# Performance work log

Hardware: AMD Instinct MI355X
Metric: run time of the kernel (lower is better)

The kernel has to match this reference:

```python
import jax, jax.numpy as jnp
import numpy as np

D_MODEL = 1024
NUM_HEADS = 16
HEAD_DIM = D_MODEL // NUM_HEADS


def setup_inputs() -> dict:
    key = jax.random.key(0)
    k_x, k_wqkv, k_bqkv, k_wout, k_bout = jax.random.split(key, 5)
    B, S = 2, 2048
    x = jax.random.normal(k_x, (B, S, D_MODEL), dtype=jnp.float32)
    # haiku Linear: y = x @ W + b, W shape [in, out]
    init_scale = 1.0 / np.sqrt(D_MODEL)
    W_qkv = jax.random.normal(k_wqkv, (D_MODEL, 3 * D_MODEL), dtype=jnp.float32) * init_scale
    b_qkv = jnp.zeros((3 * D_MODEL,), dtype=jnp.float32)
    W_out = jax.random.normal(k_wout, (D_MODEL, D_MODEL), dtype=jnp.float32) * init_scale
    b_out = jnp.zeros((D_MODEL,), dtype=jnp.float32)
    return {"x": x, "W_qkv": W_qkv, "b_qkv": b_qkv, "W_out": W_out, "b_out": b_out}


def reference(x, W_qkv, b_qkv, W_out, b_out):
    B, S, _ = x.shape
    qkv = x @ W_qkv + b_qkv                      # [B, S, 3*D]
    q, k, v = jnp.split(qkv, 3, axis=-1)         # each [B, S, D]
    # [B, S, D] -> [B, H, S, Hd]
    def heads(t):
        return t.reshape(B, S, NUM_HEADS, HEAD_DIM).transpose(0, 2, 1, 3)
    q, k, v = heads(q), heads(k), heads(v)
    scale = jnp.sqrt(jnp.float32(HEAD_DIM)).astype(x.dtype)
    attn = jnp.einsum('bhqd,bhkd->bhqk', q, k) / scale   # [B, H, S, S]
    attn = jax.nn.softmax(attn, axis=-1)
    out = jnp.einsum('bhqk,bhkd->bhqd', attn, v)          # [B, H, S, Hd]
    out = out.transpose(0, 2, 1, 3).reshape(B, S, D_MODEL)
    return out @ W_out + b_out
```

## Files before the change

### kernel.cpp

```cpp
#include <hip/hip_runtime.h>
#include <stdint.h>


#define BATCH 2
#define SEQ 2048
#define DM 1024
#define NH 16
#define HD 64
#define M_TOT 4096
#define QSCALE 0.18033688011112042f

typedef __bf16 bf16x8 __attribute__((ext_vector_type(8)));
typedef __bf16 bf16x4 __attribute__((ext_vector_type(4)));
typedef float  f32x4  __attribute__((ext_vector_type(4)));

__device__ __forceinline__ void gld_lds16(const void* g, void* l) {
    __builtin_amdgcn_global_load_lds(
        (const __attribute__((address_space(1))) uint32_t*)g,
        (__attribute__((address_space(3))) uint32_t*)l, 16, 0, 0);
}

__device__ __forceinline__ int swz(int r, int c) {
    return r * 64 + ((((c >> 3) ^ (r & 7))) << 3) + (c & 7);
}

__launch_bounds__(256)
__global__ void split_x_kernel(const float* __restrict__ x, __bf16* __restrict__ xs)
{
    const int i  = blockIdx.x * 256 + threadIdx.x;
    const int m  = i >> 8;
    const int c4 = (i & 255) * 4;
    float4 v = *reinterpret_cast<const float4*>(&x[(size_t)m * DM + c4]);
    float a[4] = {v.x, v.y, v.z, v.w};
    bf16x4 hi, lo;
    #pragma unroll
    for (int j = 0; j < 4; ++j) {
        __bf16 h = (__bf16)a[j];
        hi[j] = h;
        lo[j] = (__bf16)(a[j] - (float)h);
    }
    *reinterpret_cast<bf16x4*>(&xs[(size_t)m * (2*DM) + c4]) = hi;
    *reinterpret_cast<bf16x4*>(&xs[(size_t)m * (2*DM) + DM + c4]) = lo;
}

__launch_bounds__(256)
__global__ void split_wt_kernel(const float* __restrict__ W, __bf16* __restrict__ Wt, int N)
{
    __shared__ float T[64][69];
    const int tid = threadIdx.x;
    const int k0 = blockIdx.x * 64, n0 = blockIdx.y * 64;

    {
        const int kr = tid >> 4, c4 = (tid & 15) * 4;
        #pragma unroll
        for (int i = 0; i < 4; ++i) {
            float4 v = *reinterpret_cast<const float4*>(
                &W[(size_t)(k0 + kr + 16 * i) * N + n0 + c4]);
            *reinterpret_cast<float4*>(&T[kr + 16 * i][c4]) = v;
        }
    }
    __syncthreads();
    {
        const int n = tid >> 2, kc = (tid & 3) * 16;
        __bf16 hi[16], lo[16];
        #pragma unroll
        for (int j = 0; j < 16; ++j) {
            float v = T[kc + j][n];
            __bf16 h = (__bf16)v;
            hi[j] = h;
            lo[j] = (__bf16)(v - (float)h);
        }
        const size_t ro = (size_t)(n0 + n) * (2*DM) + k0 + kc;
        *reinterpret_cast<bf16x8*>(&Wt[ro])          = *reinterpret_cast<bf16x8*>(&hi[0]);
        *reinterpret_cast<bf16x8*>(&Wt[ro + 8])      = *reinterpret_cast<bf16x8*>(&hi[8]);
        *reinterpret_cast<bf16x8*>(&Wt[ro + DM])     = *reinterpret_cast<bf16x8*>(&lo[0]);
        *reinterpret_cast<bf16x8*>(&Wt[ro + DM + 8]) = *reinterpret_cast<bf16x8*>(&lo[8]);
    }
}

__launch_bounds__(256)
__global__ void gemm_qkv_kernel(const __bf16* __restrict__ A,
                                const __bf16* __restrict__ Bt,
                                const float* __restrict__ bias,
                                __bf16* __restrict__ qs,
                                __bf16* __restrict__ khi_g,
                                __bf16* __restrict__ klo_g,
                                __bf16* __restrict__ vt_g)
{
    __shared__ __align__(16) __bf16 pool[18432];
    __bf16* As = pool;
    __bf16* Bs = pool + 4096;

    const int tid  = threadIdx.x;
    const int w    = tid >> 6;
    const int lane = tid & 63;
    const int n16  = lane & 15;
    const int quad = lane >> 4;
    const int bm = blockIdx.x * 128, bn = blockIdx.y * 128;
    const int wm = (w & 1) * 64,     wn = (w >> 1) * 64;

    const int srow = tid >> 2, sc = (tid & 3) * 8;
    const __bf16* Ar = A  + (size_t)(bm + srow) * (2*DM) + sc;
    const __bf16* Br = Bt + (size_t)(bn + srow) * (2*DM) + sc;

    f32x4 acc[4][4] = {};

    for (int kb = 0; kb < 3 * DM; kb += 32) {
        const int a_k = (kb < DM)     ? kb : kb - DM;
        const int b_k = (kb < 2 * DM) ? kb : kb - 2 * DM;
        __syncthreads();
        gld_lds16(Ar + a_k,                    &As[(size_t)tid * 8]);
        gld_lds16(Ar + a_k + (size_t)64*2*DM,  &As[(size_t)(256 + tid) * 8]);
        gld_lds16(Br + b_k,                    &Bs[(size_t)tid * 8]);
        gld_lds16(Br + b_k + (size_t)64*2*DM,  &Bs[(size_t)(256 + tid) * 8]);
        __syncthreads();

        bf16x8 af[4], bfr[4];
        #pragma unroll
        for (int i = 0; i < 4; ++i)
            af[i] = *reinterpret_cast<const bf16x8*>(&As[(wm + i*16 + n16) * 32 + quad * 8]);
        #pragma unroll
        for (int j = 0; j < 4; ++j)
            bfr[j] = *reinterpret_cast<const bf16x8*>(&Bs[(wn + j*16 + n16) * 32 + quad * 8]);
        #pragma unroll
        for (int i = 0; i < 4; ++i)
            #pragma unroll
            for (int j = 0; j < 4; ++j)
                acc[i][j] = __builtin_amdgcn_mfma_f32_16x16x32_bf16(af[i], bfr[j], acc[i][j], 0, 0, 0);
    }

    const int colb = bn + wn;
    const int part = colb >> 10;
    const int hh   = (colb & 1023) >> 6;
    const int brow = bm + wm;
    const int b    = brow >> 11;
    const int s0   = brow & 2047;
    const int bh   = b * NH + hh;
    const int kt   = s0 >> 6;
    const size_t tb = ((size_t)bh * 32 + kt) * 4096;

    float bv[4];
    #pragma unroll
    for (int j = 0; j < 4; ++j) bv[j] = bias[colb + j * 16 + n16];

    __bf16* scrH = pool + w * 4608;
    __bf16* scrL = scrH + 2304;
    const int lr = lane & 31, hc = lane >> 5;

    __syncthreads();

    #pragma unroll
    for (int p = 0; p < 2; ++p) {
        if (part == 2) {
            #pragma unroll
            for (int jj = 0; jj < 2; ++jj) {
                const int j = 2 * p + jj;
                #pragma unroll
                for (int i = 0; i < 4; ++i) {
                    bf16x4 v4;
                    #pragma unroll
                    for (int r = 0; r < 4; ++r)
                        v4[r] = (__bf16)(acc[i][j][r] + bv[j]);
                    *reinterpret_cast<bf16x4*>(
                        &scrH[(jj * 16 + n16) * 72 + i * 16 + quad * 4]) = v4;
                }
            }
        } else {
            #pragma unroll
            for (int ii = 0; ii < 2; ++ii) {
                const int i = 2 * p + ii;
                #pragma unroll
                for (int j = 0; j < 4; ++j) {
                    #pragma unroll
                    for (int r = 0; r < 4; ++r) {
                        float val = acc[i][j][r] + bv[j];
                        if (part == 0) val *= QSCALE;
                        __bf16 h = (__bf16)val;
                        const int so = (ii * 16 + quad * 4 + r) * 72 + j * 16 + n16;
                        scrH[so] = h;
                        scrL[so] = (__bf16)(val - (float)h);
                    }
                }
            }
        }
        __syncthreads();

        if (part == 0) {
            const size_t qbase = ((size_t)bh * SEQ + s0 + 32 * p + lr) * 128;
            #pragma unroll
            for (int t = 0; t < 4; ++t) {
                const int ch = hc * 4 + t;
                *reinterpret_cast<bf16x8*>(&qs[qbase + ch * 8]) =
                    *reinterpret_cast<const bf16x8*>(&scrH[lr * 72 + ch * 8]);
                *reinterpret_cast<bf16x8*>(&qs[qbase + 64 + ch * 8]) =
                    *reinterpret_cast<const bf16x8*>(&scrL[lr * 72 + ch * 8]);
            }
        } else if (part == 1) {
            const int kr = 32 * p + lr;
            #pragma unroll
            for (int t = 0; t < 4; ++t) {
                const int ch = hc * 4 + t;
                const int src = (ch ^ (lr & 7)) * 8;
                *reinterpret_cast<bf16x8*>(&khi_g[tb + kr * 64 + ch * 8]) =
                    *reinterpret_cast<const bf16x8*>(&scrH[lr * 72 + src]);
                *reinterpret_cast<bf16x8*>(&klo_g[tb + kr * 64 + ch * 8]) =
                    *reinterpret_cast<const bf16x8*>(&scrL[lr * 72 + src]);
            }
        } else {
            const int d = 32 * p + lr;
            #pragma unroll
            for (int t = 0; t < 4; ++t) {
                const int ch = hc * 4 + t;
                const int src = (ch ^ (lr & 7)) * 8;
                *reinterpret_cast<bf16x8*>(&vt_g[tb + d * 64 + ch * 8]) =
                    *reinterpret_cast<const bf16x8*>(&scrH[lr * 72 + src]);
            }
        }
        __syncthreads();
    }
}

__launch_bounds__(256)
__global__ void gemm_out_kernel(const __bf16* __restrict__ A,
                                const __bf16* __restrict__ Bt,
                                const float* __restrict__ bias,
                                float* __restrict__ out)
{
    __shared__ __align__(16) __bf16 As[128 * 32];
    __shared__ __align__(16) __bf16 Bs[64 * 32];

    const int tid  = threadIdx.x;
    const int w    = tid >> 6;
    const int lane = tid & 63;
    const int n16  = lane & 15;
    const int quad = lane >> 4;
    const int bm = blockIdx.x * 128, bn = blockIdx.y * 64;
    const int wm = (w & 1) * 64,     wn = (w >> 1) * 32;

    const int srow = tid >> 2, sc = (tid & 3) * 8;
    const __bf16* Ar = A  + (size_t)(bm + srow) * (2*DM) + sc;
    const __bf16* Br = Bt + (size_t)(bn + srow) * (2*DM) + sc;

    f32x4 acc[4][2] = {};

    for (int kb = 0; kb < 3 * DM; kb += 32) {
        const int a_k = (kb < DM)     ? kb : kb - DM;
        const int b_k = (kb < 2 * DM) ? kb : kb - 2 * DM;
        __syncthreads();
        gld_lds16(Ar + a_k,                    &As[(size_t)tid * 8]);
        gld_lds16(Ar + a_k + (size_t)64*2*DM,  &As[(size_t)(256 + tid) * 8]);
        gld_lds16(Br + b_k,                    &Bs[(size_t)tid * 8]);
        __syncthreads();

        bf16x8 af[4], bfr[2];
        #pragma unroll
        for (int i = 0; i < 4; ++i)
            af[i] = *reinterpret_cast<const bf16x8*>(&As[(wm + i*16 + n16) * 32 + quad * 8]);
        #pragma unroll
        for (int j = 0; j < 2; ++j)
            bfr[j] = *reinterpret_cast<const bf16x8*>(&Bs[(wn + j*16 + n16) * 32 + quad * 8]);
        #pragma unroll
        for (int i = 0; i < 4; ++i)
            #pragma unroll
            for (int j = 0; j < 2; ++j)
                acc[i][j] = __builtin_amdgcn_mfma_f32_16x16x32_bf16(af[i], bfr[j], acc[i][j], 0, 0, 0);
    }

    #pragma unroll
    for (int j = 0; j < 2; ++j) {
        const int col = bn + wn + j * 16 + n16;
        const float bvv = bias[col];
        #pragma unroll
        for (int i = 0; i < 4; ++i) {
            const int row0 = bm + wm + i * 16 + quad * 4;
            #pragma unroll
            for (int r = 0; r < 4; ++r)
                out[(size_t)(row0 + r) * DM + col] = acc[i][j][r] + bvv;
        }
    }
}

__launch_bounds__(512)
__global__ void flash_attn_dma_kernel(const __bf16* __restrict__ qs,
                                      const __bf16* __restrict__ khi_g,
                                      const __bf16* __restrict__ klo_g,
                                      const __bf16* __restrict__ vt_g,
                                      __bf16* __restrict__ ctx2)
{
    __shared__ __align__(16) __bf16 Khi[4096];
    __shared__ __align__(16) __bf16 Klo[4096];
    __shared__ __align__(16) __bf16 Vt [4096];
    __shared__ __align__(16) __bf16 Ps [8192];

    const int tid  = threadIdx.x;
    const int w    = tid >> 6;
    const int lane = tid & 63;
    const int n16  = lane & 15;
    const int quad = lane >> 4;
    const int bid  = blockIdx.x;
    const int bh = (bid & 7) * 4 + (bid >> 7);
    const int qt = (bid >> 3) & 15;

    const size_t qrow = ((size_t)bh * SEQ + qt * 128 + w * 16 + n16) * 128;
    bf16x8 qh[2], ql[2];
    #pragma unroll
    for (int s2 = 0; s2 < 2; ++s2) {
        qh[s2] = *reinterpret_cast<const bf16x8*>(&qs[qrow + s2 * 32 + quad * 8]);
        ql[s2] = *reinterpret_cast<const bf16x8*>(&qs[qrow + 64 + s2 * 32 + quad * 8]);
    }

    f32x4 o[4] = {};
    float l_lane = 0.f;

    const int prow = w * 16 + n16;

    for (int kt = 0; kt < 32; ++kt) {
        const size_t tb = ((size_t)bh * 32 + kt) * 4096;
        __syncthreads();
        #pragma unroll
        for (int t = 0; t < 3; ++t) {
            const int ch = w * 3 + t;
            const int arr = ch >> 3, sub = ch & 7;
            const int eo = sub * 512 + lane * 8;
            const __bf16* g = (arr == 0 ? khi_g : arr == 1 ? klo_g : vt_g) + tb + eo;
            __bf16* l = (arr == 0 ? Khi : arr == 1 ? Klo : Vt) + eo;
            gld_lds16(g, l);
        }
        __syncthreads();

        f32x4 st[4] = {};
        #pragma unroll
        for (int kg = 0; kg < 4; ++kg) {
            const int r = kg * 16 + n16;
            #pragma unroll
            for (int s2 = 0; s2 < 2; ++s2) {
                const int off = r * 64 + (((s2 * 4 + quad) ^ (r & 7)) << 3);
                bf16x8 kh = *reinterpret_cast<const bf16x8*>(&Khi[off]);
                bf16x8 kl = *reinterpret_cast<const bf16x8*>(&Klo[off]);
                st[kg] = __builtin_amdgcn_mfma_f32_16x16x32_bf16(kh, qh[s2], st[kg], 0, 0, 0);
                st[kg] = __builtin_amdgcn_mfma_f32_16x16x32_bf16(kh, ql[s2], st[kg], 0, 0, 0);
                st[kg] = __builtin_amdgcn_mfma_f32_16x16x32_bf16(kl, qh[s2], st[kg], 0, 0, 0);
            }
        }

        float lp[4];
        #pragma unroll
        for (int kg = 0; kg < 4; ++kg) {
            f32x4 pp;
            #pragma unroll
            for (int r2 = 0; r2 < 4; ++r2)
                pp[r2] = exp2f(st[kg][r2]);
            st[kg] = pp;
            lp[kg] = (pp[0] + pp[1]) + (pp[2] + pp[3]);
        }
        l_lane += (lp[0] + lp[1]) + (lp[2] + lp[3]);

        #pragma unroll
        for (int kg = 0; kg < 4; ++kg) {
            bf16x4 p4;
            #pragma unroll
            for (int r2 = 0; r2 < 4; ++r2) p4[r2] = (__bf16)st[kg][r2];
            const int ch = kg * 2 + (quad >> 1);
            const int off = prow * 64 + ((ch ^ (prow & 7)) << 3) + (quad & 1) * 4;
            *reinterpret_cast<bf16x4*>(&Ps[off]) = p4;
        }

        bf16x8 pa[2];
        #pragma unroll
        for (int s2 = 0; s2 < 2; ++s2)
            pa[s2] = *reinterpret_cast<const bf16x8*>(
                &Ps[prow * 64 + (((s2 * 4 + quad) ^ (prow & 7)) << 3)]);
        #pragma unroll
        for (int c = 0; c < 4; ++c) {
            const int vr = c * 16 + n16;
            #pragma unroll
            for (int s2 = 0; s2 < 2; ++s2) {
                bf16x8 vb = *reinterpret_cast<const bf16x8*>(
                    &Vt[vr * 64 + (((s2 * 4 + quad) ^ (vr & 7)) << 3)]);
                o[c] = __builtin_amdgcn_mfma_f32_16x16x32_bf16(pa[s2], vb, o[c], 0, 0, 0);
            }
        }
    }

    l_lane += __shfl_xor(l_lane, 16, 64);
    l_lane += __shfl_xor(l_lane, 32, 64);

    const int b = bh >> 4, hh = bh & 15;
    #pragma unroll
    for (int r2 = 0; r2 < 4; ++r2) {
        const float l = __shfl(l_lane, (quad << 4) + quad * 4 + r2, 64);
        const float linv = 1.0f / l;
        const int srow = qt * 128 + w * 16 + quad * 4 + r2;
        const size_t rowoff = (size_t)(b * SEQ + srow) * (2*DM);
        #pragma unroll
        for (int c = 0; c < 4; ++c) {
            const int col = hh * HD + c * 16 + n16;
            float v = o[c][r2] * linv;
            __bf16 h = (__bf16)v;
            ctx2[rowoff + col] = h;
            ctx2[rowoff + DM + col] = (__bf16)(v - (float)h);
        }
    }
}

extern "C" void kernel_launch(void* const* d_in, const int* in_sizes, int n_in,
                              void* d_out, int out_size, void* d_ws, size_t ws_size,
                              hipStream_t stream)
{
    const float* x    = (const float*)d_in[0];
    const float* Wqkv = (const float*)d_in[1];
    const float* bqkv = (const float*)d_in[2];
    const float* Wout = (const float*)d_in[3];
    const float* bout = (const float*)d_in[4];
    float* out = (float*)d_out;

    char* ws = (char*)d_ws;
    __bf16* xs   = (__bf16*)(ws);
    __bf16* ctx2 = xs;
    __bf16* wqt  = (__bf16*)(ws + (size_t)16 * 1024 * 1024);
    __bf16* wot  = (__bf16*)(ws + (size_t)28 * 1024 * 1024);
    __bf16* qsb  = (__bf16*)(ws + (size_t)32 * 1024 * 1024);
    __bf16* khi  = (__bf16*)(ws + (size_t)48 * 1024 * 1024);
    __bf16* klo  = (__bf16*)(ws + (size_t)56 * 1024 * 1024);
    __bf16* vt   = (__bf16*)(ws + (size_t)64 * 1024 * 1024);

    split_x_kernel<<<dim3(M_TOT * (DM / 4) / 256), 256, 0, stream>>>(x, xs);
    split_wt_kernel<<<dim3(DM / 64, (3 * DM) / 64), 256, 0, stream>>>(Wqkv, wqt, 3 * DM);
    split_wt_kernel<<<dim3(DM / 64, DM / 64), 256, 0, stream>>>(Wout, wot, DM);

    gemm_qkv_kernel<<<dim3(M_TOT / 128, (3 * DM) / 128), 256, 0, stream>>>(
        xs, wqt, bqkv, qsb, khi, klo, vt);
    flash_attn_dma_kernel<<<dim3(512), 512, 0, stream>>>(qsb, khi, klo, vt, ctx2);
    gemm_out_kernel<<<dim3(M_TOT / 128, DM / 64), 256, 0, stream>>>(
        ctx2, wot, bout, out);
}
```

Baseline: 306.1 us.

## Give each attention wave four query groups and merge prep kernels into one launch

The flash attention kernel drops from 8 to 2 waves per block, and each wave now handles 64 query rows (four 16-row groups). Every K and V fragment read from LDS is reused across four MFMA groups, which cuts LDS read traffic per MFMA. The cost is much higher register pressure (accumulators and Q fragments for four groups), fewer waves per CU, and more DMA issues per wave. The three preprocessing kernels (x split and both weight transpose/splits) are also merged into one launch to save launch overhead.

```diff
diff --git a/kernel.cpp b/kernel.cpp
--- a/kernel.cpp
+++ b/kernel.cpp
@@ -25,30 +25,40 @@
 }
 
 __launch_bounds__(256)
-__global__ void split_x_kernel(const float* __restrict__ x, __bf16* __restrict__ xs)
-{
-    const int i  = blockIdx.x * 256 + threadIdx.x;
-    const int m  = i >> 8;
-    const int c4 = (i & 255) * 4;
-    float4 v = *reinterpret_cast<const float4*>(&x[(size_t)m * DM + c4]);
-    float a[4] = {v.x, v.y, v.z, v.w};
-    bf16x4 hi, lo;
-    #pragma unroll
-    for (int j = 0; j < 4; ++j) {
-        __bf16 h = (__bf16)a[j];
-        hi[j] = h;
-        lo[j] = (__bf16)(a[j] - (float)h);
-    }
-    *reinterpret_cast<bf16x4*>(&xs[(size_t)m * (2*DM) + c4]) = hi;
-    *reinterpret_cast<bf16x4*>(&xs[(size_t)m * (2*DM) + DM + c4]) = lo;
-}
-
-__launch_bounds__(256)
-__global__ void split_wt_kernel(const float* __restrict__ W, __bf16* __restrict__ Wt, int N)
+__global__ void prep_kernel(const float* __restrict__ x,
+                            const float* __restrict__ Wqkv,
+                            const float* __restrict__ Wout,
+                            __bf16* __restrict__ xs,
+                            __bf16* __restrict__ wqt,
+                            __bf16* __restrict__ wot)
 {
     __shared__ float T[64][69];
     const int tid = threadIdx.x;
-    const int k0 = blockIdx.x * 64, n0 = blockIdx.y * 64;
+    const int blk = blockIdx.x;
+
+    if (blk < 4096) {
+        const int i  = blk * 256 + tid;
+        const int m  = i >> 8;
+        const int c4 = (i & 255) * 4;
+        float4 v = *reinterpret_cast<const float4*>(&x[(size_t)m * DM + c4]);
+        float a[4] = {v.x, v.y, v.z, v.w};
+        bf16x4 hi, lo;
+        #pragma unroll
+        for (int j = 0; j < 4; ++j) {
+            __bf16 h = (__bf16)a[j];
+            hi[j] = h;
+            lo[j] = (__bf16)(a[j] - (float)h);
+        }
+        *reinterpret_cast<bf16x4*>(&xs[(size_t)m * (2*DM) + c4]) = hi;
+        *reinterpret_cast<bf16x4*>(&xs[(size_t)m * (2*DM) + DM + c4]) = lo;
+        return;
+    }
+
+    const int bb = (blk < 4864) ? blk - 4096 : blk - 4864;
+    const float* W = (blk < 4864) ? Wqkv : Wout;
+    __bf16* Wt     = (blk < 4864) ? wqt  : wot;
+    const int N    = (blk < 4864) ? 3 * DM : DM;
+    const int k0 = (bb & 15) * 64, n0 = (bb >> 4) * 64;
 
     {
         const int kr = tid >> 4, c4 = (tid & 15) * 4;
@@ -280,12 +290,12 @@
     }
 }
 
-__launch_bounds__(512)
-__global__ void flash_attn_dma_kernel(const __bf16* __restrict__ qs,
-                                      const __bf16* __restrict__ khi_g,
-                                      const __bf16* __restrict__ klo_g,
-                                      const __bf16* __restrict__ vt_g,
-                                      __bf16* __restrict__ ctx2)
+__launch_bounds__(128, 2)
+__global__ void flash_attn_v3_kernel(const __bf16* __restrict__ qs,
+                                     const __bf16* __restrict__ khi_g,
+                                     const __bf16* __restrict__ klo_g,
+                                     const __bf16* __restrict__ vt_g,
+                                     __bf16* __restrict__ ctx2)
 {
     __shared__ __align__(16) __bf16 Khi[4096];
     __shared__ __align__(16) __bf16 Klo[4096];
@@ -301,25 +311,27 @@
     const int bh = (bid & 7) * 4 + (bid >> 7);
     const int qt = (bid >> 3) & 15;
 
-    const size_t qrow = ((size_t)bh * SEQ + qt * 128 + w * 16 + n16) * 128;
-    bf16x8 qh[2], ql[2];
-    #pragma unroll
-    for (int s2 = 0; s2 < 2; ++s2) {
-        qh[s2] = *reinterpret_cast<const bf16x8*>(&qs[qrow + s2 * 32 + quad * 8]);
-        ql[s2] = *reinterpret_cast<const bf16x8*>(&qs[qrow + 64 + s2 * 32 + quad * 8]);
-    }
-
-    f32x4 o[4] = {};
-    float l_lane = 0.f;
-
-    const int prow = w * 16 + n16;
+    bf16x8 qh[4][2], ql[4][2];
+    #pragma unroll
+    for (int qg = 0; qg < 4; ++qg) {
+        const size_t qrow =
+            ((size_t)bh * SEQ + qt * 128 + w * 64 + qg * 16 + n16) * 128;
+        #pragma unroll
+        for (int s2 = 0; s2 < 2; ++s2) {
+            qh[qg][s2] = *reinterpret_cast<const bf16x8*>(&qs[qrow + s2 * 32 + quad * 8]);
+            ql[qg][s2] = *reinterpret_cast<const bf16x8*>(&qs[qrow + 64 + s2 * 32 + quad * 8]);
+        }
+    }
+
+    f32x4 o[4][4] = {};
+    float l_lane[4] = {};
 
     for (int kt = 0; kt < 32; ++kt) {
         const size_t tb = ((size_t)bh * 32 + kt) * 4096;
         __syncthreads();
         #pragma unroll
-        for (int t = 0; t < 3; ++t) {
-            const int ch = w * 3 + t;
+        for (int t = 0; t < 12; ++t) {
+            const int ch = w * 12 + t;
             const int arr = ch >> 3, sub = ch & 7;
             const int eo = sub * 512 + lane * 8;
             const __bf16* g = (arr == 0 ? khi_g : arr == 1 ? klo_g : vt_g) + tb + eo;
@@ -328,77 +340,87 @@
         }
         __syncthreads();
 
-        f32x4 st[4] = {};
         #pragma unroll
         for (int kg = 0; kg < 4; ++kg) {
             const int r = kg * 16 + n16;
-            #pragma unroll
-            for (int s2 = 0; s2 < 2; ++s2) {
-                const int off = r * 64 + (((s2 * 4 + quad) ^ (r & 7)) << 3);
-                bf16x8 kh = *reinterpret_cast<const bf16x8*>(&Khi[off]);
-                bf16x8 kl = *reinterpret_cast<const bf16x8*>(&Klo[off]);
-                st[kg] = __builtin_amdgcn_mfma_f32_16x16x32_bf16(kh, qh[s2], st[kg], 0, 0, 0);
-                st[kg] = __builtin_amdgcn_mfma_f32_16x16x32_bf16(kh, ql[s2], st[kg], 0, 0, 0);
-                st[kg] = __builtin_amdgcn_mfma_f32_16x16x32_bf16(kl, qh[s2], st[kg], 0, 0, 0);
-            }
-        }
-
-        float lp[4];
-        #pragma unroll
-        for (int kg = 0; kg < 4; ++kg) {
-            f32x4 pp;
-            #pragma unroll
-            for (int r2 = 0; r2 < 4; ++r2)
-                pp[r2] = exp2f(st[kg][r2]);
-            st[kg] = pp;
-            lp[kg] = (pp[0] + pp[1]) + (pp[2] + pp[3]);
-        }
-        l_lane += (lp[0] + lp[1]) + (lp[2] + lp[3]);
-
-        #pragma unroll
-        for (int kg = 0; kg < 4; ++kg) {
-            bf16x4 p4;
-            #pragma unroll
-            for (int r2 = 0; r2 < 4; ++r2) p4[r2] = (__bf16)st[kg][r2];
-            const int ch = kg * 2 + (quad >> 1);
-            const int off = prow * 64 + ((ch ^ (prow & 7)) << 3) + (quad & 1) * 4;
-            *reinterpret_cast<bf16x4*>(&Ps[off]) = p4;
-        }
-
-        bf16x8 pa[2];
-        #pragma unroll
-        for (int s2 = 0; s2 < 2; ++s2)
-            pa[s2] = *reinterpret_cast<const bf16x8*>(
-                &Ps[prow * 64 + (((s2 * 4 + quad) ^ (prow & 7)) << 3)]);
+            const int o0 = r * 64 + ((quad ^ (r & 7)) << 3);
+            const int o1 = r * 64 + (((4 + quad) ^ (r & 7)) << 3);
+            bf16x8 kh0 = *reinterpret_cast<const bf16x8*>(&Khi[o0]);
+            bf16x8 kl0 = *reinterpret_cast<const bf16x8*>(&Klo[o0]);
+            bf16x8 kh1 = *reinterpret_cast<const bf16x8*>(&Khi[o1]);
+            bf16x8 kl1 = *reinterpret_cast<const bf16x8*>(&Klo[o1]);
+            #pragma unroll
+            for (int qg = 0; qg < 4; ++qg) {
+                f32x4 st = {};
+                st = __builtin_amdgcn_mfma_f32_16x16x32_bf16(kh0, qh[qg][0], st, 0, 0, 0);
+                st = __builtin_amdgcn_mfma_f32_16x16x32_bf16(kl0, qh[qg][0], st, 0, 0, 0);
+                st = __builtin_amdgcn_mfma_f32_16x16x32_bf16(kh0, ql[qg][0], st, 0, 0, 0);
+                st = __builtin_amdgcn_mfma_f32_16x16x32_bf16(kh1, qh[qg][1], st, 0, 0, 0);
+                st = __builtin_amdgcn_mfma_f32_16x16x32_bf16(kl1, qh[qg][1], st, 0, 0, 0);
+                st = __builtin_amdgcn_mfma_f32_16x16x32_bf16(kh1, ql[qg][1], st, 0, 0, 0);
+
+                f32x4 pp;
+                #pragma unroll
+                for (int r2 = 0; r2 < 4; ++r2) pp[r2] = exp2f(st[r2]);
+                l_lane[qg] += (pp[0] + pp[1]) + (pp[2] + pp[3]);
+
+                bf16x4 p4;
+                #pragma unroll
+                for (int r2 = 0; r2 < 4; ++r2) p4[r2] = (__bf16)pp[r2];
+                const int prow = w * 64 + qg * 16 + n16;
+                const int ch2 = kg * 2 + (quad >> 1);
+                const int off = prow * 64 + ((ch2 ^ (prow & 7)) << 3) + (quad & 1) * 4;
+                *reinterpret_cast<bf16x4*>(&Ps[off]) = p4;
+            }
+        }
+
+        bf16x8 pa[4][2];
+        #pragma unroll
+        for (int qg = 0; qg < 4; ++qg) {
+            const int prow = w * 64 + qg * 16 + n16;
+            #pragma unroll
+            for (int s2 = 0; s2 < 2; ++s2)
+                pa[qg][s2] = *reinterpret_cast<const bf16x8*>(
+                    &Ps[prow * 64 + (((s2 * 4 + quad) ^ (prow & 7)) << 3)]);
+        }
         #pragma unroll
         for (int c = 0; c < 4; ++c) {
             const int vr = c * 16 + n16;
-            #pragma unroll
-            for (int s2 = 0; s2 < 2; ++s2) {
-                bf16x8 vb = *reinterpret_cast<const bf16x8*>(
-                    &Vt[vr * 64 + (((s2 * 4 + quad) ^ (vr & 7)) << 3)]);
-                o[c] = __builtin_amdgcn_mfma_f32_16x16x32_bf16(pa[s2], vb, o[c], 0, 0, 0);
-            }
-        }
-    }
-
-    l_lane += __shfl_xor(l_lane, 16, 64);
-    l_lane += __shfl_xor(l_lane, 32, 64);
+            bf16x8 vb0 = *reinterpret_cast<const bf16x8*>(
+                &Vt[vr * 64 + ((quad ^ (vr & 7)) << 3)]);
+            bf16x8 vb1 = *reinterpret_cast<const bf16x8*>(
+                &Vt[vr * 64 + (((4 + quad) ^ (vr & 7)) << 3)]);
+            #pragma unroll
+            for (int qg = 0; qg < 4; ++qg) {
+                o[qg][c] = __builtin_amdgcn_mfma_f32_16x16x32_bf16(pa[qg][0], vb0, o[qg][c], 0, 0, 0);
+                o[qg][c] = __builtin_amdgcn_mfma_f32_16x16x32_bf16(pa[qg][1], vb1, o[qg][c], 0, 0, 0);
+            }
+        }
+    }
+
+    #pragma unroll
+    for (int qg = 0; qg < 4; ++qg) {
+        l_lane[qg] += __shfl_xor(l_lane[qg], 16, 64);
+        l_lane[qg] += __shfl_xor(l_lane[qg], 32, 64);
+    }
 
     const int b = bh >> 4, hh = bh & 15;
     #pragma unroll
-    for (int r2 = 0; r2 < 4; ++r2) {
-        const float l = __shfl(l_lane, (quad << 4) + quad * 4 + r2, 64);
-        const float linv = 1.0f / l;
-        const int srow = qt * 128 + w * 16 + quad * 4 + r2;
-        const size_t rowoff = (size_t)(b * SEQ + srow) * (2*DM);
-        #pragma unroll
-        for (int c = 0; c < 4; ++c) {
-            const int col = hh * HD + c * 16 + n16;
-            float v = o[c][r2] * linv;
-            __bf16 h = (__bf16)v;
-            ctx2[rowoff + col] = h;
-            ctx2[rowoff + DM + col] = (__bf16)(v - (float)h);
+    for (int qg = 0; qg < 4; ++qg) {
+        #pragma unroll
+        for (int r2 = 0; r2 < 4; ++r2) {
+            const float l = __shfl(l_lane[qg], (quad << 4) + quad * 4 + r2, 64);
+            const float linv = 1.0f / l;
+            const int srow = qt * 128 + w * 64 + qg * 16 + quad * 4 + r2;
+            const size_t rowoff = (size_t)(b * SEQ + srow) * (2*DM);
+            #pragma unroll
+            for (int c = 0; c < 4; ++c) {
+                const int col = hh * HD + c * 16 + n16;
+                float v = o[qg][c][r2] * linv;
+                __bf16 h = (__bf16)v;
+                ctx2[rowoff + col] = h;
+                ctx2[rowoff + DM + col] = (__bf16)(v - (float)h);
+            }
         }
     }
 }
@@ -424,13 +446,10 @@
     __bf16* klo  = (__bf16*)(ws + (size_t)56 * 1024 * 1024);
     __bf16* vt   = (__bf16*)(ws + (size_t)64 * 1024 * 1024);
 
-    split_x_kernel<<<dim3(M_TOT * (DM / 4) / 256), 256, 0, stream>>>(x, xs);
-    split_wt_kernel<<<dim3(DM / 64, (3 * DM) / 64), 256, 0, stream>>>(Wqkv, wqt, 3 * DM);
-    split_wt_kernel<<<dim3(DM / 64, DM / 64), 256, 0, stream>>>(Wout, wot, DM);
-
+    prep_kernel<<<dim3(5120), 256, 0, stream>>>(x, Wqkv, Wout, xs, wqt, wot);
     gemm_qkv_kernel<<<dim3(M_TOT / 128, (3 * DM) / 128), 256, 0, stream>>>(
         xs, wqt, bqkv, qsb, khi, klo, vt);
-    flash_attn_dma_kernel<<<dim3(512), 512, 0, stream>>>(qsb, khi, klo, vt, ctx2);
+    flash_attn_v3_kernel<<<dim3(512), 128, 0, stream>>>(qsb, khi, klo, vt, ctx2);
     gemm_out_kernel<<<dim3(M_TOT / 128, DM / 64), 256, 0, stream>>>(
         ctx2, wot, bout, out);
 }
```

Measured after the change: 353.9 us. 15.6% more time.
